# Optimization experiments

Measured on AMD Instinct MI355X. Metric: run time of the kernel, lower is better.

## Reference

```python
import jax, jax.numpy as jnp
from jax import lax
import numpy as np

K = 7          # kernel size
PAD = 3        # (K-1)//2
KK = K * K     # 49 taps


def setup_inputs() -> dict:
    key = jax.random.key(0)
    ks = jax.random.split(key, 5)
    B, C, H, W = 8, 256, 128, 128
    x = jax.random.normal(ks[0], (B, C, H, W), jnp.float32)
    # conv_offset: Conv2d(2, 3*KK, k=7, pad=3). Small init so offsets are modest.
    w_off = jax.random.normal(ks[1], (3 * KK, 2, K, K), jnp.float32) * 0.01
    b_off = jax.random.normal(ks[2], (3 * KK,), jnp.float32) * 0.01
    # DCN weight: Conv2d(2, 1, k=7)
    w_dcn = jax.random.normal(ks[3], (1, 2, K, K), jnp.float32) * (1.0 / np.sqrt(2 * KK))
    b_dcn = jnp.zeros((1,), jnp.float32)
    bn_gamma = jnp.ones((1,), jnp.float32)
    bn_beta = jnp.zeros((1,), jnp.float32)
    bn_mean = jnp.zeros((1,), jnp.float32)
    bn_var = jnp.ones((1,), jnp.float32)
    return {"x": x, "w_off": w_off, "b_off": b_off, "w_dcn": w_dcn,
            "b_dcn": b_dcn, "bn_gamma": bn_gamma, "bn_beta": bn_beta,
            "bn_mean": bn_mean, "bn_var": bn_var}


def _deform_spatial_att(x, w_off, b_off, w_dcn, b_dcn, bn_gamma, bn_beta, bn_mean, bn_var):
    B, C, H, W = x.shape
    dt = x.dtype
    # channel mean / max pooling -> [B, 2, H, W]
    y = jnp.concatenate([x.mean(1, keepdims=True), x.max(1, keepdims=True)], axis=1)

    # offset/mask generator conv (mmcv ModulatedDeformConv2dPack.conv_offset)
    off = lax.conv_general_dilated(y, w_off, (1, 1), [(PAD, PAD), (PAD, PAD)])
    off = off + b_off[None, :, None, None]                     # [B, 3*KK, H, W]
    o1, o2, m = off[:, :KK], off[:, KK:2 * KK], off[:, 2 * KK:]
    offset = jnp.concatenate([o1, o2], axis=1)                 # [B, 2*KK, H, W]
    dy = offset[:, 0::2]                                       # y-offset per tap, [B, KK, H, W]
    dx = offset[:, 1::2]                                       # x-offset per tap
    mask = jax.nn.sigmoid(m)                                   # modulation, [B, KK, H, W]

    # sampling locations: p = p0 + p_k + offset
    kk = jnp.arange(K, dtype=dt) - PAD
    ky = jnp.repeat(kk, K)                                     # [KK]
    kx = jnp.tile(kk, K)                                       # [KK]
    hh = jnp.arange(H, dtype=dt)
    ww = jnp.arange(W, dtype=dt)
    py = hh[None, None, :, None] + ky[None, :, None, None] + dy   # [B, KK, H, W]
    px = ww[None, None, None, :] + kx[None, :, None, None] + dx

    # bilinear sampling with zero padding outside the feature map
    y0 = jnp.floor(py)
    x0 = jnp.floor(px)
    iy0 = y0.astype(jnp.int32)
    ix0 = x0.astype(jnp.int32)
    iy1 = iy0 + 1
    ix1 = ix0 + 1
    wy1 = py - y0
    wy0 = 1.0 - wy1
    wx1 = px - x0
    wx0 = 1.0 - wx1

    y_flat = y.reshape(B, 2, H * W)

    def gather(iy, ix):
        valid = ((iy >= 0) & (iy < H) & (ix >= 0) & (ix < W))
        idx = jnp.clip(iy, 0, H - 1) * W + jnp.clip(ix, 0, W - 1)   # [B, KK, H, W]
        g = jax.vmap(lambda yb, ib: yb[:, ib])(y_flat, idx)          # [B, 2, KK, H, W]
        return g * valid[:, None].astype(dt)

    val = (gather(iy0, ix0) * (wy0 * wx0)[:, None]
           + gather(iy0, ix1) * (wy0 * wx1)[:, None]
           + gather(iy1, ix0) * (wy1 * wx0)[:, None]
           + gather(iy1, ix1) * (wy1 * wx1)[:, None])                # [B, 2, KK, H, W]

    sampled = val * mask[:, None]
    # deformable conv accumulation: 2 in-channels x 49 taps -> 1 out-channel
    out = jnp.einsum('bckhw,ck->bhw', sampled, w_dcn[0].reshape(2, KK)) + b_dcn
    out = out[:, None]                                               # [B, 1, H, W]

    # BatchNorm2d(1), inference-mode normalization
    eps = 1e-5
    out = (out - bn_mean[None, :, None, None]) * (bn_gamma[None, :, None, None]
          * lax.rsqrt(bn_var[None, :, None, None] + eps)) + bn_beta[None, :, None, None]

    gate = jax.nn.sigmoid(out)                                       # [B, 1, H, W]
    return jnp.broadcast_to(gate, x.shape)


def reference(x, w_off, b_off, w_dcn, b_dcn, bn_gamma, bn_beta, bn_mean, bn_var):
    return _deform_spatial_att(x, w_off, b_off, w_dcn, b_dcn,
                               bn_gamma, bn_beta, bn_mean, bn_var)
```

## Files before the change

### kernel.cpp

```cpp
#include <hip/hip_runtime.h>
#include <cstdint>

#define BB 8
#define CC 256
#define HH 128
#define WW 128
#define HW (HH * WW)

typedef __attribute__((ext_vector_type(8))) short bf16x8;
typedef __attribute__((ext_vector_type(4))) float f32x4;

__global__ __launch_bounds__(512) void reduce_meanmax(const float* __restrict__ x,
                                                      float* __restrict__ y2) {
    const int bh = blockIdx.x;
    const int b  = bh >> 7;
    const int h  = bh & 127;
    const int t  = threadIdx.x;
    const int wq = t & 31;
    const int cg = t >> 5;

    const float* xb = x + ((size_t)(b * CC + cg * 16) * HH + h) * WW;

    float4 s = make_float4(0.f, 0.f, 0.f, 0.f);
    float4 m = make_float4(-INFINITY, -INFINITY, -INFINITY, -INFINITY);
    #pragma unroll 4
    for (int i = 0; i < 16; ++i) {
        float4 v = ((const float4*)(xb + (size_t)i * HW))[wq];
        s.x += v.x; s.y += v.y; s.z += v.z; s.w += v.w;
        m.x = fmaxf(m.x, v.x); m.y = fmaxf(m.y, v.y);
        m.z = fmaxf(m.z, v.z); m.w = fmaxf(m.w, v.w);
    }

    __shared__ float4 ls[16][32];
    __shared__ float4 lm[16][32];
    ls[cg][wq] = s;
    lm[cg][wq] = m;
    __syncthreads();

    if (t < 32) {
        float4 S = ls[0][t];
        float4 M = lm[0][t];
        #pragma unroll
        for (int g = 1; g < 16; ++g) {
            float4 a = ls[g][t];
            float4 c = lm[g][t];
            S.x += a.x; S.y += a.y; S.z += a.z; S.w += a.w;
            M.x = fmaxf(M.x, c.x); M.y = fmaxf(M.y, c.y);
            M.z = fmaxf(M.z, c.z); M.w = fmaxf(M.w, c.w);
        }
        const float inv = 1.0f / 256.0f;
        float4 o0 = make_float4(S.x * inv, M.x, S.y * inv, M.y);
        float4 o1 = make_float4(S.z * inv, M.z, S.w * inv, M.w);
        float4* yo = (float4*)(y2 + ((size_t)b * HW + (size_t)h * WW) * 2);
        yo[2 * t]     = o0;
        yo[2 * t + 1] = o1;
    }
}

__device__ __forceinline__ uint32_t f2bf(float f) {
    uint32_t u = __float_as_uint(f);
    return (u + 0x7FFFu + ((u >> 16) & 1u)) >> 16;
}
__device__ __forceinline__ float bf2f(uint32_t u) {
    return __uint_as_float(u << 16);
}

__global__ __launch_bounds__(256) void prep_B(const float* __restrict__ w_off,
                                              uint16_t* __restrict__ Bpre) {
    const int idx = blockIdx.x * 256 + threadIdx.x;
    if (idx >= 4 * 4 * 160 * 8) return;
    const int e  = idx & 7;
    const int t1 = idx >> 3;
    const int j  = t1 % 160;
    const int t2 = t1 / 160;
    const int g  = t2 & 3;
    const int kt = t2 >> 2;
    const int k  = kt * 32 + g * 8 + e;
    uint16_t v = 0;
    if (k < 98 && j < 147) {
        const int ch = (j < 49) ? (2 * j) : ((j < 98) ? (2 * (j - 49) + 1) : j);
        v = (uint16_t)f2bf(w_off[(size_t)ch * 98 + k]);
    }
    Bpre[idx] = v;
}

__global__ __launch_bounds__(256) void deform_gate(
    const float* __restrict__ y2, const uint16_t* __restrict__ Bpre,
    const float* __restrict__ b_off,
    const float* __restrict__ w_dcn, const float* __restrict__ b_dcn,
    const float* __restrict__ bn_gamma, const float* __restrict__ bn_beta,
    const float* __restrict__ bn_mean, const float* __restrict__ bn_var,
    float* __restrict__ out)
{
    const int bid  = blockIdx.x;
    const int rowg = bid >> 2;
    const int qpos = (bid & 3) * 32;
    const int b = rowg >> 7;
    const int h = rowg & 127;
    const int t = threadIdx.x;
    const int wv = t >> 6;
    const int l  = t & 63;
    const int mhalf = wv >> 1;
    const int nhalf = wv & 1;
    const bool act = (l < 49);
    const int ls = act ? l : 0;

    __shared__ uint32_t patch_pk[7][40];
    __shared__ uint16_t cv[2][16][168];
    __shared__ float gate_blk[32];

    const float2* y2b = (const float2*)y2 + (size_t)b * HW;

    for (int i = t; i < 7 * 40; i += 256) {
        const int r  = i / 40;
        const int xi = i % 40;
        const int xx = qpos + xi - 3;
        const int yy = h + r - 3;
        uint32_t v = 0;
        if (yy >= 0 && yy < HH && xx >= 0 && xx < WW) {
            float2 g2 = y2b[yy * WW + xx];
            v = f2bf(g2.x) | (f2bf(g2.y) << 16);
        }
        patch_pk[r][xi] = v;
    }

    const float b_dy = b_off[2 * ls];
    const float b_dx = b_off[2 * ls + 1];
    const float b_m  = b_off[98 + ls];
    const float wd0 = w_dcn[ls];
    const float wd1 = w_dcn[49 + ls];
    const int kr = ls / 7;
    const int kc = ls % 7;
    const float bscale = bn_gamma[0] * rsqrtf(bn_var[0] + 1e-5f);
    const float gB = (b_dcn[0] - bn_mean[0]) * bscale + bn_beta[0];

    __syncthreads();

    const int m = l & 15;
    const int g = l >> 4;
    const int plocal = mhalf * 16 + m;
    const uint16_t* patch_u16 = (const uint16_t*)patch_pk;

    f32x4 acc[5];
    #pragma unroll
    for (int nn = 0; nn < 5; ++nn) acc[nn] = (f32x4){0.f, 0.f, 0.f, 0.f};

    #pragma unroll
    for (int kt = 0; kt < 4; ++kt) {
        union { uint16_t u[8]; bf16x8 v; } af;
        const int K0 = kt * 32 + g * 8;
        #pragma unroll
        for (int e = 0; e < 8; ++e) {
            const int k  = K0 + e;
            const int kk = (k < 98) ? k : 0;
            const int ci = (kk >= 49) ? 1 : 0;
            const int rc = kk - 49 * ci;
            const int r  = rc / 7;
            const int c  = rc - 7 * r;
            const uint16_t val = patch_u16[(r * 40 + plocal + c) * 2 + ci];
            af.u[e] = (k < 98) ? val : (uint16_t)0;
        }
        #pragma unroll
        for (int nn = 0; nn < 5; ++nn) {
            const int j = (nhalf * 5 + nn) * 16 + m;
            const bf16x8 bfr = *(const bf16x8*)(Bpre + (((kt * 4 + g) * 160 + j) << 3));
            acc[nn] = __builtin_amdgcn_mfma_f32_16x16x32_bf16(af.v, bfr, acc[nn], 0, 0, 0);
        }
    }

    #pragma unroll
    for (int nn = 0; nn < 5; ++nn) {
        #pragma unroll
        for (int q = 0; q < 4; ++q) {
            cv[mhalf][g * 4 + q][(nhalf * 5 + nn) * 16 + m] = (uint16_t)f2bf(acc[nn][q]);
        }
    }
    __syncthreads();

    const uint16_t* cvp = &cv[0][0][0];
    #pragma unroll 4
    for (int pi = 0; pi < 8; ++pi) {
        const int pp = wv * 8 + pi;
        const int posn = qpos + pp;
        const int cbase = pp * 168;

        const float dyv = bf2f(cvp[cbase + ls])      + b_dy;
        const float dxv = bf2f(cvp[cbase + 49 + ls]) + b_dx;
        const float mv  = bf2f(cvp[cbase + 98 + ls]) + b_m;
        const float mk = 1.0f / (1.0f + __expf(-mv));

        const float fy = (float)(h + kr - 3) + dyv;
        const float fx = (float)(posn + kc - 3) + dxv;
        const float fly = floorf(fy), flx = floorf(fx);
        const int iy0 = (int)fly, ix0 = (int)flx;
        const int iy1 = iy0 + 1,  ix1 = ix0 + 1;
        const float wy1 = fy - fly, wy0 = 1.0f - wy1;
        const float wx1 = fx - flx, wx0 = 1.0f - wx1;

        const float vy0 = (iy0 >= 0 && iy0 < HH) ? 1.0f : 0.0f;
        const float vy1 = (iy1 >= 0 && iy1 < HH) ? 1.0f : 0.0f;
        const float vx0 = (ix0 >= 0 && ix0 < WW) ? 1.0f : 0.0f;
        const float vx1 = (ix1 >= 0 && ix1 < WW) ? 1.0f : 0.0f;

        const int cy0 = min(max(iy0, 0), HH - 1) * WW;
        const int cy1 = min(max(iy1, 0), HH - 1) * WW;
        const int cx0 = min(max(ix0, 0), WW - 1);
        const int cx1 = min(max(ix1, 0), WW - 1);

        const float w00 = wy0 * wx0 * vy0 * vx0;
        const float w01 = wy0 * wx1 * vy0 * vx1;
        const float w10 = wy1 * wx0 * vy1 * vx0;
        const float w11 = wy1 * wx1 * vy1 * vx1;

        const float2 g00 = y2b[cy0 + cx0];
        const float2 g01 = y2b[cy0 + cx1];
        const float2 g10 = y2b[cy1 + cx0];
        const float2 g11 = y2b[cy1 + cx1];

        const float v0s = g00.x * w00 + g01.x * w01 + g10.x * w10 + g11.x * w11;
        const float v1s = g00.y * w00 + g01.y * w01 + g10.y * w10 + g11.y * w11;

        float tval = mk * fmaf(v0s, wd0, v1s * wd1);
        tval = act ? tval : 0.0f;

        float ssum = tval;
        #pragma unroll
        for (int off = 1; off < 64; off <<= 1)
            ssum += __shfl_xor(ssum, off);

        if (l == 0) {
            const float o = ssum * bscale + gB;
            gate_blk[pp] = 1.0f / (1.0f + __expf(-o));
        }
    }

    __syncthreads();

    const size_t ob = (size_t)b * CC * HW + (size_t)h * WW + qpos;
    const f32x4* gb4 = (const f32x4*)gate_blk;
    #pragma unroll
    for (int it = 0; it < 8; ++it) {
        const int idx = it * 256 + t;
        const int c   = idx >> 3;
        const int q4  = idx & 7;
        __builtin_nontemporal_store(gb4[q4], (f32x4*)(out + ob + (size_t)c * HW) + q4);
    }
}

extern "C" void kernel_launch(void* const* d_in, const int* in_sizes, int n_in,
                              void* d_out, int out_size, void* d_ws, size_t ws_size,
                              hipStream_t stream) {
    const float* x        = (const float*)d_in[0];
    const float* w_off    = (const float*)d_in[1];
    const float* b_off    = (const float*)d_in[2];
    const float* w_dcn    = (const float*)d_in[3];
    const float* b_dcn    = (const float*)d_in[4];
    const float* bn_gamma = (const float*)d_in[5];
    const float* bn_beta  = (const float*)d_in[6];
    const float* bn_mean  = (const float*)d_in[7];
    const float* bn_var   = (const float*)d_in[8];
    float* out = (float*)d_out;

    float*    y2   = (float*)d_ws;
    uint16_t* Bpre = (uint16_t*)((char*)d_ws + (1 << 20));

    prep_B<<<(4 * 4 * 160 * 8 + 255) / 256, 256, 0, stream>>>(w_off, Bpre);
    reduce_meanmax<<<BB * HH, 512, 0, stream>>>(x, y2);
    deform_gate<<<4 * BB * HH, 256, 0, stream>>>(y2, Bpre, b_off, w_dcn, b_dcn,
                                                 bn_gamma, bn_beta, bn_mean, bn_var,
                                                 out);
}
```

Measured before the change: 74.57 us.

## Use zero-padded y2 buffers to remove bounds checks in patch load and bilinear gather

The mean/max reduction now writes into two zero-padded workspace layouts: an fp32 float2 grid with a one-pixel halo, and a packed bf16 grid with a three-pixel halo. The patch load in deform_gate becomes a branch-free copy, and the bilinear gather clamps indices into the halo instead of computing validity masks. prep_B is enlarged to 512 blocks so it also zeroes the padded buffers on every call. This adds a zeroing pass and a second write of the reduced map, which is a little extra memory traffic in exchange for simpler inner loops.

```diff
diff --git a/kernel.cpp b/kernel.cpp
--- a/kernel.cpp
+++ b/kernel.cpp
@@ -7,11 +7,50 @@
 #define WW 128
 #define HW (HH * WW)
 
+#define G_STRIDE 130
+#define P_ROWS 134
+#define P_STRIDE 140
+#define Y2G_BYTES ((size_t)BB * G_STRIDE * G_STRIDE * 8)
+#define Y2P_BYTES ((size_t)BB * P_ROWS * P_STRIDE * 4)
+
 typedef __attribute__((ext_vector_type(8))) short bf16x8;
 typedef __attribute__((ext_vector_type(4))) float f32x4;
 
+__device__ __forceinline__ uint32_t f2bf(float f) {
+    uint32_t u = __float_as_uint(f);
+    return (u + 0x7FFFu + ((u >> 16) & 1u)) >> 16;
+}
+__device__ __forceinline__ float bf2f(uint32_t u) {
+    return __uint_as_float(u << 16);
+}
+
+__global__ __launch_bounds__(256) void prep_B(const float* __restrict__ w_off,
+                                              uint16_t* __restrict__ Bpre,
+                                              uint32_t* __restrict__ zbase) {
+    const int gid = blockIdx.x * 256 + threadIdx.x;
+    if (gid < 4 * 4 * 160 * 8) {
+        const int e  = gid & 7;
+        const int t1 = gid >> 3;
+        const int j  = t1 % 160;
+        const int t2 = t1 / 160;
+        const int g  = t2 & 3;
+        const int kt = t2 >> 2;
+        const int k  = kt * 32 + g * 8 + e;
+        uint16_t v = 0;
+        if (k < 98 && j < 147) {
+            const int ch = (j < 49) ? (2 * j) : ((j < 98) ? (2 * (j - 49) + 1) : j);
+            v = (uint16_t)f2bf(w_off[(size_t)ch * 98 + k]);
+        }
+        Bpre[gid] = v;
+    }
+    const int ztot = (int)((Y2G_BYTES + Y2P_BYTES) / 4);
+    for (int i = gid; i < ztot; i += gridDim.x * 256)
+        zbase[i] = 0;
+}
+
 __global__ __launch_bounds__(512) void reduce_meanmax(const float* __restrict__ x,
-                                                      float* __restrict__ y2) {
+                                                      float* __restrict__ y2g,
+                                                      uint32_t* __restrict__ y2p) {
     const int bh = blockIdx.x;
     const int b  = bh >> 7;
     const int h  = bh & 127;
@@ -49,43 +88,22 @@
             M.z = fmaxf(M.z, c.z); M.w = fmaxf(M.w, c.w);
         }
         const float inv = 1.0f / 256.0f;
-        float4 o0 = make_float4(S.x * inv, M.x, S.y * inv, M.y);
-        float4 o1 = make_float4(S.z * inv, M.z, S.w * inv, M.w);
-        float4* yo = (float4*)(y2 + ((size_t)b * HW + (size_t)h * WW) * 2);
-        yo[2 * t]     = o0;
-        yo[2 * t + 1] = o1;
-    }
-}
-
-__device__ __forceinline__ uint32_t f2bf(float f) {
-    uint32_t u = __float_as_uint(f);
-    return (u + 0x7FFFu + ((u >> 16) & 1u)) >> 16;
-}
-__device__ __forceinline__ float bf2f(uint32_t u) {
-    return __uint_as_float(u << 16);
-}
-
-__global__ __launch_bounds__(256) void prep_B(const float* __restrict__ w_off,
-                                              uint16_t* __restrict__ Bpre) {
-    const int idx = blockIdx.x * 256 + threadIdx.x;
-    if (idx >= 4 * 4 * 160 * 8) return;
-    const int e  = idx & 7;
-    const int t1 = idx >> 3;
-    const int j  = t1 % 160;
-    const int t2 = t1 / 160;
-    const int g  = t2 & 3;
-    const int kt = t2 >> 2;
-    const int k  = kt * 32 + g * 8 + e;
-    uint16_t v = 0;
-    if (k < 98 && j < 147) {
-        const int ch = (j < 49) ? (2 * j) : ((j < 98) ? (2 * (j - 49) + 1) : j);
-        v = (uint16_t)f2bf(w_off[(size_t)ch * 98 + k]);
-    }
-    Bpre[idx] = v;
+        const float mn[4] = {S.x * inv, S.y * inv, S.z * inv, S.w * inv};
+        const float mx[4] = {M.x, M.y, M.z, M.w};
+
+        float2* gr = (float2*)y2g + ((size_t)b * G_STRIDE + (h + 1)) * G_STRIDE + (4 * t + 1);
+        uint32_t* pr = y2p + ((size_t)(b * P_ROWS) + (h + 3)) * P_STRIDE + (4 * t + 3);
+        #pragma unroll
+        for (int q = 0; q < 4; ++q) {
+            gr[q] = make_float2(mn[q], mx[q]);
+            pr[q] = f2bf(mn[q]) | (f2bf(mx[q]) << 16);
+        }
+    }
 }
 
 __global__ __launch_bounds__(256) void deform_gate(
-    const float* __restrict__ y2, const uint16_t* __restrict__ Bpre,
+    const float* __restrict__ y2g, const uint32_t* __restrict__ y2p,
+    const uint16_t* __restrict__ Bpre,
     const float* __restrict__ b_off,
     const float* __restrict__ w_dcn, const float* __restrict__ b_dcn,
     const float* __restrict__ bn_gamma, const float* __restrict__ bn_beta,
@@ -109,19 +127,15 @@
     __shared__ uint16_t cv[2][16][168];
     __shared__ float gate_blk[32];
 
-    const float2* y2b = (const float2*)y2 + (size_t)b * HW;
-
-    for (int i = t; i < 7 * 40; i += 256) {
-        const int r  = i / 40;
-        const int xi = i % 40;
-        const int xx = qpos + xi - 3;
-        const int yy = h + r - 3;
-        uint32_t v = 0;
-        if (yy >= 0 && yy < HH && xx >= 0 && xx < WW) {
-            float2 g2 = y2b[yy * WW + xx];
-            v = f2bf(g2.x) | (f2bf(g2.y) << 16);
-        }
-        patch_pk[r][xi] = v;
+    const uint32_t* y2pb = y2p + (size_t)(b * P_ROWS) * P_STRIDE;
+    #pragma unroll
+    for (int i = 0; i < 2; ++i) {
+        const int idx = i * 256 + t;
+        if (idx < 7 * 40) {
+            const int r  = idx / 40;
+            const int xi = idx % 40;
+            patch_pk[r][xi] = y2pb[(h + r) * P_STRIDE + (qpos + xi)];
+        }
     }
 
     const float b_dy = b_off[2 * ls];
@@ -177,6 +191,7 @@
     }
     __syncthreads();
 
+    const float2* y2gb = (const float2*)y2g + (size_t)b * G_STRIDE * G_STRIDE;
     const uint16_t* cvp = &cv[0][0][0];
     #pragma unroll 4
     for (int pi = 0; pi < 8; ++pi) {
@@ -193,29 +208,25 @@
         const float fx = (float)(posn + kc - 3) + dxv;
         const float fly = floorf(fy), flx = floorf(fx);
         const int iy0 = (int)fly, ix0 = (int)flx;
-        const int iy1 = iy0 + 1,  ix1 = ix0 + 1;
         const float wy1 = fy - fly, wy0 = 1.0f - wy1;
         const float wx1 = fx - flx, wx0 = 1.0f - wx1;
 
-        const float vy0 = (iy0 >= 0 && iy0 < HH) ? 1.0f : 0.0f;
-        const float vy1 = (iy1 >= 0 && iy1 < HH) ? 1.0f : 0.0f;
-        const float vx0 = (ix0 >= 0 && ix0 < WW) ? 1.0f : 0.0f;
-        const float vx1 = (ix1 >= 0 && ix1 < WW) ? 1.0f : 0.0f;
-
-        const int cy0 = min(max(iy0, 0), HH - 1) * WW;
-        const int cy1 = min(max(iy1, 0), HH - 1) * WW;
-        const int cx0 = min(max(ix0, 0), WW - 1);
-        const int cx1 = min(max(ix1, 0), WW - 1);
-
-        const float w00 = wy0 * wx0 * vy0 * vx0;
-        const float w01 = wy0 * wx1 * vy0 * vx1;
-        const float w10 = wy1 * wx0 * vy1 * vx0;
-        const float w11 = wy1 * wx1 * vy1 * vx1;
-
-        const float2 g00 = y2b[cy0 + cx0];
-        const float2 g01 = y2b[cy0 + cx1];
-        const float2 g10 = y2b[cy1 + cx0];
-        const float2 g11 = y2b[cy1 + cx1];
+        const int ry0 = min(max(iy0, -1), HH) + 1;
+        const int ry1 = min(max(iy0 + 1, -1), HH) + 1;
+        const int cx0 = min(max(ix0, -1), WW) + 1;
+        const int cx1 = min(max(ix0 + 1, -1), WW) + 1;
+
+        const float2* row0 = y2gb + ry0 * G_STRIDE;
+        const float2* row1 = y2gb + ry1 * G_STRIDE;
+        const float2 g00 = row0[cx0];
+        const float2 g01 = row0[cx1];
+        const float2 g10 = row1[cx0];
+        const float2 g11 = row1[cx1];
+
+        const float w00 = wy0 * wx0;
+        const float w01 = wy0 * wx1;
+        const float w10 = wy1 * wx0;
+        const float w11 = wy1 * wx1;
 
         const float v0s = g00.x * w00 + g01.x * w01 + g10.x * w10 + g11.x * w11;
         const float v1s = g00.y * w00 + g01.y * w01 + g10.y * w10 + g11.y * w11;
@@ -261,12 +272,13 @@
     const float* bn_var   = (const float*)d_in[8];
     float* out = (float*)d_out;
 
-    float*    y2   = (float*)d_ws;
-    uint16_t* Bpre = (uint16_t*)((char*)d_ws + (1 << 20));
-
-    prep_B<<<(4 * 4 * 160 * 8 + 255) / 256, 256, 0, stream>>>(w_off, Bpre);
-    reduce_meanmax<<<BB * HH, 512, 0, stream>>>(x, y2);
-    deform_gate<<<4 * BB * HH, 256, 0, stream>>>(y2, Bpre, b_off, w_dcn, b_dcn,
-                                                 bn_gamma, bn_beta, bn_mean, bn_var,
-                                                 out);
-}
+    float*    y2g  = (float*)d_ws;
+    uint32_t* y2p  = (uint32_t*)((char*)d_ws + Y2G_BYTES);
+    uint16_t* Bpre = (uint16_t*)((char*)d_ws + Y2G_BYTES + Y2P_BYTES + 256);
+
+    prep_B<<<512, 256, 0, stream>>>(w_off, Bpre, (uint32_t*)d_ws);
+    reduce_meanmax<<<BB * HH, 512, 0, stream>>>(x, y2g, y2p);
+    deform_gate<<<4 * BB * HH, 256, 0, stream>>>(y2g, y2p, Bpre, b_off,
+                                                 w_dcn, b_dcn, bn_gamma, bn_beta,
+                                                 bn_mean, bn_var, out);
+}
```

Measured after the change: 79.27 us. 1.06x slower.

## Fold weight prep into reduction kernel and reorganize K layout for contiguous A-fragment loads

Applied to the files above, without the earlier changes.

The separate prep_B launch is removed, and each reduction block now writes a slice of the bf16 weight matrix. The weight matrix is reordered so that each group of 8 K entries holds one kernel row (7 taps plus a zero pad). In the gate kernel the mean and max patches are stored as separate bf16 planes with padding rows. Each A fragment can then be built from five 32-bit LDS reads and funnel shifts, replacing eight scattered 16-bit loads with index arithmetic. This saves a kernel launch and reduces LDS address computation, but it couples the weight prep to the reduction kernel and requires the new K ordering to match exactly.

```diff
diff --git a/kernel.cpp b/kernel.cpp
--- a/kernel.cpp
+++ b/kernel.cpp
@@ -10,15 +10,40 @@
 typedef __attribute__((ext_vector_type(8))) short bf16x8;
 typedef __attribute__((ext_vector_type(4))) float f32x4;
 
+__device__ __forceinline__ uint32_t f2bf(float f) {
+    uint32_t u = __float_as_uint(f);
+    return (u + 0x7FFFu + ((u >> 16) & 1u)) >> 16;
+}
+__device__ __forceinline__ float bf2f(uint32_t u) {
+    return __uint_as_float(u << 16);
+}
+
 __global__ __launch_bounds__(512) void reduce_meanmax(const float* __restrict__ x,
-                                                      float* __restrict__ y2) {
+                                                      float* __restrict__ y2,
+                                                      const float* __restrict__ w_off,
+                                                      uint16_t* __restrict__ Bpre) {
     const int bh = blockIdx.x;
     const int b  = bh >> 7;
     const int h  = bh & 127;
     const int t  = threadIdx.x;
+
+    if (t < 20) {
+        const int idx = bh * 20 + t;
+        const int e   = idx & 7;
+        const int t1  = idx >> 3;
+        const int j   = t1 % 160;
+        const int grp = t1 / 160;
+        uint16_t v = 0;
+        if (grp < 14 && e < 7 && j < 147) {
+            const int ci = grp / 7, r = grp % 7;
+            const int ch = (j < 49) ? (2 * j) : ((j < 98) ? (2 * (j - 49) + 1) : j);
+            v = (uint16_t)f2bf(w_off[(size_t)ch * 98 + ci * 49 + r * 7 + e]);
+        }
+        Bpre[idx] = v;
+    }
+
     const int wq = t & 31;
     const int cg = t >> 5;
-
     const float* xb = x + ((size_t)(b * CC + cg * 16) * HH + h) * WW;
 
     float4 s = make_float4(0.f, 0.f, 0.f, 0.f);
@@ -55,33 +80,6 @@
         yo[2 * t]     = o0;
         yo[2 * t + 1] = o1;
     }
-}
-
-__device__ __forceinline__ uint32_t f2bf(float f) {
-    uint32_t u = __float_as_uint(f);
-    return (u + 0x7FFFu + ((u >> 16) & 1u)) >> 16;
-}
-__device__ __forceinline__ float bf2f(uint32_t u) {
-    return __uint_as_float(u << 16);
-}
-
-__global__ __launch_bounds__(256) void prep_B(const float* __restrict__ w_off,
-                                              uint16_t* __restrict__ Bpre) {
-    const int idx = blockIdx.x * 256 + threadIdx.x;
-    if (idx >= 4 * 4 * 160 * 8) return;
-    const int e  = idx & 7;
-    const int t1 = idx >> 3;
-    const int j  = t1 % 160;
-    const int t2 = t1 / 160;
-    const int g  = t2 & 3;
-    const int kt = t2 >> 2;
-    const int k  = kt * 32 + g * 8 + e;
-    uint16_t v = 0;
-    if (k < 98 && j < 147) {
-        const int ch = (j < 49) ? (2 * j) : ((j < 98) ? (2 * (j - 49) + 1) : j);
-        v = (uint16_t)f2bf(w_off[(size_t)ch * 98 + k]);
-    }
-    Bpre[idx] = v;
 }
 
 __global__ __launch_bounds__(256) void deform_gate(
@@ -105,7 +103,7 @@
     const bool act = (l < 49);
     const int ls = act ? l : 0;
 
-    __shared__ uint32_t patch_pk[7][40];
+    __shared__ uint16_t patch2[16][48];
     __shared__ uint16_t cv[2][16][168];
     __shared__ float gate_blk[32];
 
@@ -116,13 +114,17 @@
         const int xi = i % 40;
         const int xx = qpos + xi - 3;
         const int yy = h + r - 3;
-        uint32_t v = 0;
+        uint32_t mn = 0, mx = 0;
         if (yy >= 0 && yy < HH && xx >= 0 && xx < WW) {
             float2 g2 = y2b[yy * WW + xx];
-            v = f2bf(g2.x) | (f2bf(g2.y) << 16);
-        }
-        patch_pk[r][xi] = v;
-    }
+            mn = f2bf(g2.x);
+            mx = f2bf(g2.y);
+        }
+        patch2[r][xi]     = (uint16_t)mn;
+        patch2[7 + r][xi] = (uint16_t)mx;
+    }
+    for (int i = t; i < 2 * 48; i += 256)
+        patch2[14 + (i / 48)][i % 48] = 0;
 
     const float b_dy = b_off[2 * ls];
     const float b_dx = b_off[2 * ls + 1];
@@ -139,7 +141,7 @@
     const int m = l & 15;
     const int g = l >> 4;
     const int plocal = mhalf * 16 + m;
-    const uint16_t* patch_u16 = (const uint16_t*)patch_pk;
+    const uint32_t* p32 = (const uint32_t*)&patch2[0][0];
 
     f32x4 acc[5];
     #pragma unroll
@@ -147,23 +149,20 @@
 
     #pragma unroll
     for (int kt = 0; kt < 4; ++kt) {
-        union { uint16_t u[8]; bf16x8 v; } af;
-        const int K0 = kt * 32 + g * 8;
-        #pragma unroll
-        for (int e = 0; e < 8; ++e) {
-            const int k  = K0 + e;
-            const int kk = (k < 98) ? k : 0;
-            const int ci = (kk >= 49) ? 1 : 0;
-            const int rc = kk - 49 * ci;
-            const int r  = rc / 7;
-            const int c  = rc - 7 * r;
-            const uint16_t val = patch_u16[(r * 40 + plocal + c) * 2 + ci];
-            af.u[e] = (k < 98) ? val : (uint16_t)0;
-        }
+        const int grp = kt * 4 + g;
+        const int W   = grp * 48 + plocal;
+        const uint32_t sh8 = (W & 1) ? 16u : 0u;
+        const uint32_t* dp = p32 + (W >> 1);
+        const uint32_t d0 = dp[0], d1 = dp[1], d2 = dp[2], d3 = dp[3], d4 = dp[4];
+        union { uint32_t u[4]; bf16x8 v; } af;
+        af.u[0] = (uint32_t)(((((uint64_t)d1) << 32) | d0) >> sh8);
+        af.u[1] = (uint32_t)(((((uint64_t)d2) << 32) | d1) >> sh8);
+        af.u[2] = (uint32_t)(((((uint64_t)d3) << 32) | d2) >> sh8);
+        af.u[3] = (uint32_t)(((((uint64_t)d4) << 32) | d3) >> sh8);
         #pragma unroll
         for (int nn = 0; nn < 5; ++nn) {
             const int j = (nhalf * 5 + nn) * 16 + m;
-            const bf16x8 bfr = *(const bf16x8*)(Bpre + (((kt * 4 + g) * 160 + j) << 3));
+            const bf16x8 bfr = *(const bf16x8*)(Bpre + ((grp * 160 + j) << 3));
             acc[nn] = __builtin_amdgcn_mfma_f32_16x16x32_bf16(af.v, bfr, acc[nn], 0, 0, 0);
         }
     }
@@ -264,8 +263,7 @@
     float*    y2   = (float*)d_ws;
     uint16_t* Bpre = (uint16_t*)((char*)d_ws + (1 << 20));
 
-    prep_B<<<(4 * 4 * 160 * 8 + 255) / 256, 256, 0, stream>>>(w_off, Bpre);
-    reduce_meanmax<<<BB * HH, 512, 0, stream>>>(x, y2);
+    reduce_meanmax<<<BB * HH, 512, 0, stream>>>(x, y2, w_off, Bpre);
     deform_gate<<<4 * BB * HH, 256, 0, stream>>>(y2, Bpre, b_off, w_dcn, b_dcn,
                                                  bn_gamma, bn_beta, bn_mean, bn_var,
                                                  out);
```

Result: faster. 69.12 us (-7.3%).
